# Kernel tuning notes

Hardware: AMD Instinct MI355X
Metric: run time of the kernel (lower is better)

## Reference

```python
import jax, jax.numpy as jnp
import numpy as np

K = 7          # kernel_size
PAD = ((K - 1) * (1 - 1) + K) // 2  # = 3, 'same' padding for dilation=1


def setup_inputs() -> dict:
    key = jax.random.key(0)
    k1, k2 = jax.random.split(key)
    x = jax.random.normal(k1, (16, 96, 128, 128), dtype=jnp.float32)
    weight = jax.random.normal(k2, (96, K, K), dtype=jnp.float32) * 0.1
    return {"x": x, "weight": weight}


def reference(x, weight):
    """Morphological dilation2d with soft_max=True (ReLU after).

    Equivalent to torch: unfold(x, K, padding=PAD) -> max over window of
    (patch + w). nn.Unfold zero-pads, so borders see literal zeros in the max;
    we reproduce that with jnp.pad (zeros), not -inf padding.
    """
    B, C, H, W = x.shape
    xp = jnp.pad(x, ((0, 0), (0, 0), (PAD, PAD), (PAD, PAD)))  # zero pad, matches nn.Unfold
    out = jnp.full((B, C, H, W), -jnp.inf, dtype=x.dtype)
    # Fixed K*K loop over kernel taps (structural, not data-dim loop):
    # running max avoids materializing the (B,H*W,C,K*K) im2col tensor.
    for i in range(K):
        for j in range(K):
            shifted = jax.lax.dynamic_slice(xp, (0, 0, i, j), (B, C, H, W))
            out = jnp.maximum(out, shifted + weight[None, :, i, j, None, None])
    return jax.nn.relu(out)  # soft_max=True -> ReLU activation
```

## Files before the change

### kernel.cpp

```cpp
#include <hip/hip_runtime.h>

#define HH 128
#define WW 128
#define CC 96
#define KK 7

struct Row { float4 a, b, c; };

__device__ __forceinline__ float elem(const Row& r, int k) {
  switch (k) {
    case 0:  return r.a.x; case 1:  return r.a.y; case 2:  return r.a.z; case 3:  return r.a.w;
    case 4:  return r.b.x; case 5:  return r.b.y; case 6:  return r.b.z; case 7:  return r.b.w;
    case 8:  return r.c.x; case 9:  return r.c.y; case 10: return r.c.z; default: return r.c.w;
  }
}

__device__ __forceinline__ Row load_row(const float* __restrict__ xp, int r,
                                        int tc0, bool lok, bool rok) {
  Row o;
  const float4 z = make_float4(0.f, 0.f, 0.f, 0.f);
  if ((unsigned)r < (unsigned)HH) {
    const float* p = xp + r * WW + tc0 - 4;
    o.a = lok ? *(const float4*)(p)     : z;
    o.b =       *(const float4*)(p + 4);
    o.c = rok ? *(const float4*)(p + 8) : z;
  } else {
    o.a = z; o.b = z; o.c = z;
  }
  return o;
}

__device__ __forceinline__ float tapq(const Row& r, int q, const float* wr) {
  float t0 = elem(r, q + 1) + wr[0];
  float t1 = elem(r, q + 2) + wr[1];
  float t2 = elem(r, q + 3) + wr[2];
  float t3 = elem(r, q + 4) + wr[3];
  float t4 = elem(r, q + 5) + wr[4];
  float t5 = elem(r, q + 6) + wr[5];
  float t6 = elem(r, q + 7) + wr[6];
  float u0 = fmaxf(fmaxf(t0, t1), t2);
  float u1 = fmaxf(fmaxf(t3, t4), t5);
  return fmaxf(fmaxf(u0, u1), t6);
}

#define TAP_ROW(R, I)                             \
  m0 = fmaxf(m0, tapq(R, 0, wv + (I)*7));        \
  m1 = fmaxf(m1, tapq(R, 1, wv + (I)*7));        \
  m2 = fmaxf(m2, tapq(R, 2, wv + (I)*7));        \
  m3 = fmaxf(m3, tapq(R, 3, wv + (I)*7));

__global__ __launch_bounds__(256, 2) void morph_kernel(
    const float* __restrict__ x, const float* __restrict__ weight,
    float* __restrict__ out) {
  const int t = threadIdx.x;
  const int cg = t & 31;
  const int rg = t >> 5;
  const int half = blockIdx.x & 1;
  const int plane = blockIdx.x >> 1;
  const int c = plane % CC;

  const float* __restrict__ xp = x + (size_t)plane * (HH * WW);
  float* __restrict__ op = out + (size_t)plane * (HH * WW);
  const float* __restrict__ Wc = weight + c * (KK * KK);

  float wv[KK * KK];
#pragma unroll
  for (int k = 0; k < KK * KK; ++k)
    wv[k] = __int_as_float(__builtin_amdgcn_readfirstlane(__float_as_int(Wc[k])));

  const int tc0 = cg << 2;
  const int row0 = half * 64 + rg * 8;
  const bool lok = (tc0 >= 4);
  const bool rok = (tc0 <= WW - 8);

  Row r0 = load_row(xp, row0 - 3, tc0, lok, rok);
  Row r1 = load_row(xp, row0 - 2, tc0, lok, rok);
  Row r2 = load_row(xp, row0 - 1, tc0, lok, rok);
  Row r3 = load_row(xp, row0 + 0, tc0, lok, rok);
  Row r4 = load_row(xp, row0 + 1, tc0, lok, rok);
  Row r5 = load_row(xp, row0 + 2, tc0, lok, rok);

#pragma unroll
  for (int orow = 0; orow < 8; ++orow) {
    Row r6 = load_row(xp, row0 + 3 + orow, tc0, lok, rok);

    float m0 = 0.f, m1 = 0.f, m2 = 0.f, m3 = 0.f;
    TAP_ROW(r0, 0)
    TAP_ROW(r1, 1)
    TAP_ROW(r2, 2)
    TAP_ROW(r3, 3)
    TAP_ROW(r4, 4)
    TAP_ROW(r5, 5)
    TAP_ROW(r6, 6)

    *(float4*)(op + (size_t)(row0 + orow) * WW + tc0) = make_float4(m0, m1, m2, m3);

    r0 = r1; r1 = r2; r2 = r3; r3 = r4; r4 = r5; r5 = r6;
  }
}

extern "C" void kernel_launch(void* const* d_in, const int* in_sizes, int n_in,
                              void* d_out, int out_size, void* d_ws, size_t ws_size,
                              hipStream_t stream) {
  const float* x = (const float*)d_in[0];
  const float* w = (const float*)d_in[1];
  float* out = (float*)d_out;
  const int nblocks = 16 * CC * 2;
  morph_kernel<<<nblocks, 256, 0, stream>>>(x, w, out);
}
```

Baseline: 208.3 us.

## Stage padded input tile in LDS and accumulate output rows from shared memory

Each block now cooperatively loads a zero-padded 70x136 halo tile of its half-plane into shared memory, then each thread reads rows from LDS and scatters tap contributions into 8 register accumulators. This replaces redundant per-thread global loads of overlapping halo rows and the per-load bounds checks with one coalesced global read per element. Launch bounds now ask for 4 blocks per SM, which pushes register pressure up while the ~38KB tile limits occupancy. It also adds a barrier and LDS traffic.

```diff
diff --git a/kernel.cpp b/kernel.cpp
--- a/kernel.cpp
+++ b/kernel.cpp
@@ -4,6 +4,9 @@
 #define WW 128
 #define CC 96
 #define KK 7
+
+#define TROWS 70
+#define TPITCH 136
 
 struct Row { float4 a, b, c; };
 
@@ -13,21 +16,6 @@
     case 4:  return r.b.x; case 5:  return r.b.y; case 6:  return r.b.z; case 7:  return r.b.w;
     case 8:  return r.c.x; case 9:  return r.c.y; case 10: return r.c.z; default: return r.c.w;
   }
-}
-
-__device__ __forceinline__ Row load_row(const float* __restrict__ xp, int r,
-                                        int tc0, bool lok, bool rok) {
-  Row o;
-  const float4 z = make_float4(0.f, 0.f, 0.f, 0.f);
-  if ((unsigned)r < (unsigned)HH) {
-    const float* p = xp + r * WW + tc0 - 4;
-    o.a = lok ? *(const float4*)(p)     : z;
-    o.b =       *(const float4*)(p + 4);
-    o.c = rok ? *(const float4*)(p + 8) : z;
-  } else {
-    o.a = z; o.b = z; o.c = z;
-  }
-  return o;
 }
 
 __device__ __forceinline__ float tapq(const Row& r, int q, const float* wr) {
@@ -43,21 +31,18 @@
   return fmaxf(fmaxf(u0, u1), t6);
 }
 
-#define TAP_ROW(R, I)                             \
-  m0 = fmaxf(m0, tapq(R, 0, wv + (I)*7));        \
-  m1 = fmaxf(m1, tapq(R, 1, wv + (I)*7));        \
-  m2 = fmaxf(m2, tapq(R, 2, wv + (I)*7));        \
-  m3 = fmaxf(m3, tapq(R, 3, wv + (I)*7));
-
-__global__ __launch_bounds__(256, 2) void morph_kernel(
+__global__ __launch_bounds__(256, 4) void morph_kernel(
     const float* __restrict__ x, const float* __restrict__ weight,
     float* __restrict__ out) {
+  __shared__ float tile[TROWS * TPITCH];
+
   const int t = threadIdx.x;
   const int cg = t & 31;
   const int rg = t >> 5;
   const int half = blockIdx.x & 1;
   const int plane = blockIdx.x >> 1;
   const int c = plane % CC;
+  const int row_base = half * 64;
 
   const float* __restrict__ xp = x + (size_t)plane * (HH * WW);
   float* __restrict__ op = out + (size_t)plane * (HH * WW);
@@ -68,35 +53,52 @@
   for (int k = 0; k < KK * KK; ++k)
     wv[k] = __int_as_float(__builtin_amdgcn_readfirstlane(__float_as_int(Wc[k])));
 
-  const int tc0 = cg << 2;
-  const int row0 = half * 64 + rg * 8;
-  const bool lok = (tc0 >= 4);
-  const bool rok = (tc0 <= WW - 8);
+  {
+    const float4 z = make_float4(0.f, 0.f, 0.f, 0.f);
+#pragma unroll
+    for (int k = 0; k < 10; ++k) {
+      int s = t + k * 256;
+      if (s < TROWS * (TPITCH / 4)) {
+        int L  = s / (TPITCH / 4);
+        int c4 = s % (TPITCH / 4);
+        int gr = row_base - 3 + L;
+        int gc = 4 * c4 - 4;
+        bool valid = ((unsigned)gr < (unsigned)HH) & (c4 >= 1) & (c4 <= 32);
+        float4 v = valid ? *(const float4*)(xp + gr * WW + gc) : z;
+        *(float4*)(tile + L * TPITCH + 4 * c4) = v;
+      }
+    }
+  }
+  __syncthreads();
 
-  Row r0 = load_row(xp, row0 - 3, tc0, lok, rok);
-  Row r1 = load_row(xp, row0 - 2, tc0, lok, rok);
-  Row r2 = load_row(xp, row0 - 1, tc0, lok, rok);
-  Row r3 = load_row(xp, row0 + 0, tc0, lok, rok);
-  Row r4 = load_row(xp, row0 + 1, tc0, lok, rok);
-  Row r5 = load_row(xp, row0 + 2, tc0, lok, rok);
+  const float* tbase = tile + rg * 8 * TPITCH + cg * 4;
+
+  float4 m[8];
+#pragma unroll
+  for (int o = 0; o < 8; ++o) m[o] = make_float4(0.f, 0.f, 0.f, 0.f);
 
 #pragma unroll
-  for (int orow = 0; orow < 8; ++orow) {
-    Row r6 = load_row(xp, row0 + 3 + orow, tc0, lok, rok);
+  for (int L = 0; L < 14; ++L) {
+    Row r;
+    r.a = *(const float4*)(tbase + L * TPITCH);
+    r.b = *(const float4*)(tbase + L * TPITCH + 4);
+    r.c = *(const float4*)(tbase + L * TPITCH + 8);
+#pragma unroll
+    for (int o = 0; o < 8; ++o) {
+      const int i = L - o;
+      if (i >= 0 && i < KK) {
+        const float* wr = wv + i * KK;
+        m[o].x = fmaxf(m[o].x, tapq(r, 0, wr));
+        m[o].y = fmaxf(m[o].y, tapq(r, 1, wr));
+        m[o].z = fmaxf(m[o].z, tapq(r, 2, wr));
+        m[o].w = fmaxf(m[o].w, tapq(r, 3, wr));
+      }
+    }
+  }
 
-    float m0 = 0.f, m1 = 0.f, m2 = 0.f, m3 = 0.f;
-    TAP_ROW(r0, 0)
-    TAP_ROW(r1, 1)
-    TAP_ROW(r2, 2)
-    TAP_ROW(r3, 3)
-    TAP_ROW(r4, 4)
-    TAP_ROW(r5, 5)
-    TAP_ROW(r6, 6)
-
-    *(float4*)(op + (size_t)(row0 + orow) * WW + tc0) = make_float4(m0, m1, m2, m3);
-
-    r0 = r1; r1 = r2; r2 = r3; r3 = r4; r4 = r5; r5 = r6;
-  }
+#pragma unroll
+  for (int o = 0; o < 8; ++o)
+    *(float4*)(op + (size_t)(row_base + rg * 8 + o) * WW + cg * 4) = m[o];
 }
 
 extern "C" void kernel_launch(void* const* d_in, const int* in_sizes, int n_in,
```

New measurement: 210.5 us. No clear change (+1.1%).
